# Performance work log

Hardware: AMD Instinct MI355X
Metric: run time of the kernel (lower is better)

Reference implementation:

```python
import jax, jax.numpy as jnp
import numpy as np

D_MODEL = 1024
D_STATE = 16
D_CONV = 4
EXPAND = 2
D_INNER = EXPAND * D_MODEL
DT_RANK = -(-D_MODEL // 16)  # ceil(d_model/16) = 64
LN_EPS = 1e-5


def setup_inputs() -> dict:
    key = jax.random.key(0)
    ks = jax.random.split(key, 10)
    b, l = 1, 2048
    s = 0.02
    x = jax.random.normal(ks[0], (b, l, D_MODEL), dtype=jnp.float32)
    gamma = jnp.ones((D_MODEL,), jnp.float32)
    beta = jnp.zeros((D_MODEL,), jnp.float32)
    w_in = jax.random.normal(ks[1], (2 * D_INNER, D_MODEL), jnp.float32) * s
    conv_w = jax.random.normal(ks[2], (D_INNER, D_CONV), jnp.float32) * s
    conv_b = jnp.zeros((D_INNER,), jnp.float32)
    w_x = jax.random.normal(ks[3], (DT_RANK + 2 * D_STATE, D_INNER), jnp.float32) * s
    w_dt = jax.random.normal(ks[4], (D_INNER, DT_RANK), jnp.float32) * s
    b_dt = jax.random.normal(ks[5], (D_INNER,), jnp.float32) * s
    A_log = jnp.log(jnp.broadcast_to(jnp.arange(1, D_STATE + 1, dtype=jnp.float32)[None, :], (D_INNER, D_STATE)))
    Dp = jnp.ones((D_INNER,), jnp.float32)
    w_out = jax.random.normal(ks[6], (D_MODEL, D_INNER), jnp.float32) * s
    return {"x": x, "gamma": gamma, "beta": beta, "w_in": w_in, "conv_w": conv_w,
            "conv_b": conv_b, "w_x": w_x, "w_dt": w_dt, "b_dt": b_dt,
            "A_log": A_log, "Dp": Dp, "w_out": w_out}


def _combine(e1, e2):
    # (a2, b2) o (a1, b1) = (a2*a1, a2*b1 + b2); e2 is the later element
    a1, b1 = e1
    a2, b2 = e2
    return (a2 * a1, a2 * b1 + b2)


def _forward(x, gamma, beta, w_in, conv_w, conv_b, w_x, w_dt, b_dt, A_log, Dp, w_out):
    residual = x
    # LayerNorm
    mu = jnp.mean(x, axis=-1, keepdims=True)
    var = jnp.var(x, axis=-1, keepdims=True)
    xn = (x - mu) * jax.lax.rsqrt(var + LN_EPS) * gamma + beta
    # in_proj and split
    xz = jnp.einsum('bld,ed->ble', xn, w_in)
    x_part, z = xz[..., :D_INNER], xz[..., D_INNER:]
    # causal depthwise conv1d (torch pads k-1 both sides then trims to l == left pad)
    lhs = jnp.transpose(x_part, (0, 2, 1))  # (b, d_inner, l)
    rhs = conv_w[:, None, :]                # (d_inner, 1, k)
    conv = jax.lax.conv_general_dilated(
        lhs, rhs, window_strides=(1,), padding=[(D_CONV - 1, 0)],
        dimension_numbers=('NCH', 'OIH', 'NCH'), feature_group_count=D_INNER)
    x_part = jnp.transpose(conv, (0, 2, 1)) + conv_b  # (b, l, d_inner)
    x_part = jax.nn.silu(x_part)  # dropout is identity in eval mode
    # SSM
    A = -jnp.exp(A_log)  # (d_inner, n)
    x_dbl = jnp.einsum('bld,ed->ble', x_part, w_x)
    dt = x_dbl[..., :DT_RANK]
    B = x_dbl[..., DT_RANK:DT_RANK + D_STATE]
    C = x_dbl[..., DT_RANK + D_STATE:]
    delta = jax.nn.softplus(jnp.einsum('blr,dr->bld', dt, w_dt) + b_dt)  # (b,l,d_inner)
    deltaA = jnp.exp(delta[..., None] * A[None, None])                    # (b,l,d_inner,n)
    dBu = delta[..., None] * B[:, :, None, :] * x_part[..., None]         # (b,l,d_inner,n)
    _, h = jax.lax.associative_scan(_combine, (deltaA, dBu), axis=1)
    y = jnp.sum(h * C[:, :, None, :], axis=-1) + x_part * Dp             # (b,l,d_inner)
    y = y * jax.nn.silu(z)
    out = jnp.einsum('ble,de->bld', y, w_out) + residual
    return out


def reference(x, gamma, beta, w_in, conv_w, conv_b, w_x, w_dt, b_dt, A_log, Dp, w_out):
    return _forward(x, gamma, beta, w_in, conv_w, conv_b, w_x, w_dt, b_dt, A_log, Dp, w_out)
```

## Files before the change

### kernel.cpp

```cpp
#include <hip/hip_runtime.h>
#include <math.h>

#define L_SEQ 2048
#define DM 1024
#define DI 2048
#define DS 16
#define DR 64
#define XDN 96
#define NCHUNK 64
#define TCH 32
#define KSLICES 8
#define KSL (DI / KSLICES)

typedef __attribute__((ext_vector_type(8))) short bf16x8;
typedef __attribute__((ext_vector_type(4))) float f32x4;
typedef unsigned short ushort_t;
typedef __attribute__((address_space(1))) const unsigned int GU32;
typedef __attribute__((address_space(3))) unsigned int LU32;

__device__ inline unsigned short f2bf(float f) {
  unsigned int u = __builtin_bit_cast(unsigned int, f);
  u += 0x7fffu + ((u >> 16) & 1u);
  return (unsigned short)(u >> 16);
}
__device__ inline float bf2f(unsigned short u) {
  return __builtin_bit_cast(float, (unsigned int)u << 16);
}

__device__ inline void cvt4(const float* src, ushort_t* dst, int j) {
  float4 v = ((const float4*)src)[j];
  ushort4 o;
  o.x = f2bf(v.x); o.y = f2bf(v.y); o.z = f2bf(v.z); o.w = f2bf(v.w);
  ((ushort4*)dst)[j] = o;
}

__global__ void cvt_all_kernel(const float* __restrict__ w_in,
                               const float* __restrict__ w_out,
                               const float* __restrict__ w_x,
                               const float* __restrict__ w_dt,
                               ushort_t* __restrict__ w_inb,
                               ushort_t* __restrict__ w_outb,
                               ushort_t* __restrict__ w_xb,
                               ushort_t* __restrict__ w_dtb) {
  int i = blockIdx.x * 256 + threadIdx.x;
  const int N0 = 2 * DI * DM / 4;
  const int N1 = N0 + DM * DI / 4;
  const int N2 = N1 + 128 * DI / 4;
  const int N3 = N2 + DI * DR / 4;
  if (i < N0) {
    cvt4(w_in, w_inb, i);
  } else if (i < N1) {
    cvt4(w_out, w_outb, i - N0);
  } else if (i < N2) {
    int j = i - N1;
    int e0 = j << 2;
    int row = e0 >> 11;
    int col = e0 & (DI - 1);
    ushort4 o = {0, 0, 0, 0};
    if (row < XDN) {
      float4 v = *(const float4*)(w_x + (size_t)row * DI + col);
      o.x = f2bf(v.x); o.y = f2bf(v.y); o.z = f2bf(v.z); o.w = f2bf(v.w);
    }
    ((ushort4*)w_xb)[j] = o;
  } else if (i < N3) {
    cvt4(w_dt, w_dtb, i - N2);
  }
}

__global__ void ln_kernel(const float* __restrict__ x,
                          const float* __restrict__ gamma,
                          const float* __restrict__ beta,
                          ushort_t* __restrict__ xnb) {
  int row = blockIdx.x;
  int t = threadIdx.x;
  const float4* xr = (const float4*)(x + (size_t)row * DM);
  float4 v = xr[t];
  float s = v.x + v.y + v.z + v.w;
  float s2 = v.x * v.x + v.y * v.y + v.z * v.z + v.w * v.w;
#pragma unroll
  for (int off = 32; off > 0; off >>= 1) {
    s += __shfl_down(s, off);
    s2 += __shfl_down(s2, off);
  }
  __shared__ float ls[4], ls2[4];
  if ((t & 63) == 0) { ls[t >> 6] = s; ls2[t >> 6] = s2; }
  __syncthreads();
  float tot = ls[0] + ls[1] + ls[2] + ls[3];
  float tot2 = ls2[0] + ls2[1] + ls2[2] + ls2[3];
  float mu = tot * (1.0f / DM);
  float var = tot2 * (1.0f / DM) - mu * mu;
  float r = rsqrtf(var + 1e-5f);
  float4 g = ((const float4*)gamma)[t];
  float4 b = ((const float4*)beta)[t];
  ushort4 o;
  o.x = f2bf((v.x - mu) * r * g.x + b.x);
  o.y = f2bf((v.y - mu) * r * g.y + b.y);
  o.z = f2bf((v.z - mu) * r * g.z + b.z);
  o.w = f2bf((v.w - mu) * r * g.w + b.w);
  ((ushort4*)(xnb + (size_t)row * DM))[t] = o;
}

template <int EPI>
__global__ __launch_bounds__(256) void mgemm(
    const ushort_t* __restrict__ A, int lda,
    const ushort_t* __restrict__ B, int ldb,
    void* __restrict__ Cp, int ldc, int ksl,
    const float* __restrict__ extra) {
  __shared__ ushort_t As[2][128 * 64];
  __shared__ ushort_t Bs[2][128 * 64];
  const int tid = threadIdx.x;
  const int lane = tid & 63;
  const int wave = tid >> 6;
  const int m0 = blockIdx.y * 128;
  const int n0 = blockIdx.x * 128;
  const int kbase = blockIdx.z * ksl;
  const int wr = (wave >> 1) * 64;
  const int wc = (wave & 1) * 64;
  const int kq = lane >> 4;
  const int rr = lane & 15;
  f32x4 acc[4][4];
#pragma unroll
  for (int i = 0; i < 4; ++i)
#pragma unroll
    for (int j = 0; j < 4; ++j) acc[i][j] = (f32x4){0.f, 0.f, 0.f, 0.f};

  int ur[4], uc[4];
#pragma unroll
  for (int q = 0; q < 4; ++q) {
    int u = tid + 256 * q;
    ur[q] = u >> 3;
    uc[q] = (((u & 7) ^ (ur[q] & 7)) << 3);
  }

#define STAGE(K0, S)                                                          \
  do {                                                                        \
    _Pragma("unroll") for (int q = 0; q < 4; ++q)                             \
        __builtin_amdgcn_global_load_lds(                                     \
            (GU32*)(A + (size_t)(m0 + ur[q]) * lda + (K0) + uc[q]),           \
            (LU32*)(&As[S][0] + (tid + 256 * q) * 8), 16, 0, 0);              \
    _Pragma("unroll") for (int q = 0; q < 4; ++q)                             \
        __builtin_amdgcn_global_load_lds(                                     \
            (GU32*)(B + (size_t)(n0 + ur[q]) * ldb + (K0) + uc[q]),           \
            (LU32*)(&Bs[S][0] + (tid + 256 * q) * 8), 16, 0, 0);              \
  } while (0)

  const int nk = ksl >> 6;
  STAGE(kbase, 0);
  for (int t = 0; t < nk; ++t) {
    const int cur = t & 1;
    if (t + 1 < nk) {
      STAGE(kbase + (t + 1) * 64, cur ^ 1);
      asm volatile("s_waitcnt vmcnt(8)" ::: "memory");
    } else {
      asm volatile("s_waitcnt vmcnt(0)" ::: "memory");
    }
    __builtin_amdgcn_s_barrier();
#pragma unroll
    for (int kk = 0; kk < 2; ++kk) {
      const int sw = ((rr & 7) << 4);
      bf16x8 a[4], b[4];
#pragma unroll
      for (int i = 0; i < 4; ++i) {
        int row = wr + i * 16 + rr;
        int off = ((kk * 64 + kq * 16) ^ sw);
        a[i] = *(const bf16x8*)((const char*)&As[cur][0] + row * 128 + off);
      }
#pragma unroll
      for (int j = 0; j < 4; ++j) {
        int row = wc + j * 16 + rr;
        int off = ((kk * 64 + kq * 16) ^ sw);
        b[j] = *(const bf16x8*)((const char*)&Bs[cur][0] + row * 128 + off);
      }
#pragma unroll
      for (int i = 0; i < 4; ++i)
#pragma unroll
        for (int j = 0; j < 4; ++j)
          acc[i][j] = __builtin_amdgcn_mfma_f32_16x16x32_bf16(a[i], b[j], acc[i][j], 0, 0, 0);
    }
    __builtin_amdgcn_s_barrier();
  }
#undef STAGE

#pragma unroll
  for (int i = 0; i < 4; ++i) {
#pragma unroll
    for (int j = 0; j < 4; ++j) {
#pragma unroll
      for (int r = 0; r < 4; ++r) {
        int row = m0 + wr + i * 16 + kq * 4 + r;
        int col = n0 + wc + j * 16 + rr;
        float v = acc[i][j][r];
        if (EPI == 4) {
          ((ushort_t*)Cp)[(size_t)row * ldc + col] = f2bf(v);
        } else if (EPI == 5) {
          v += extra[col];
          v = (v > 20.f) ? v : __logf(1.f + __expf(v));
          ((ushort_t*)Cp)[(size_t)row * ldc + col] = f2bf(v);
        } else if (EPI == 6) {
          ((float*)Cp)[((size_t)blockIdx.z * L_SEQ + row) * ldc + col] = v;
        }
      }
    }
  }
}

__global__ void reduce_xdbl_kernel(const float* __restrict__ part,
                                   float* __restrict__ xdbl,
                                   ushort_t* __restrict__ dtb) {
  int i = blockIdx.x * 256 + threadIdx.x;
  int col = i & 127;
  int row = i >> 7;
  float s = 0.f;
#pragma unroll
  for (int k = 0; k < KSLICES; ++k) s += part[(size_t)k * (L_SEQ * 128) + i];
  if (col < DR) dtb[(size_t)row * DR + col] = f2bf(s);
  if (col < XDN) xdbl[(size_t)row * XDN + col] = s;
}

__global__ void reduce_out_kernel(const float* __restrict__ part,
                                  const float* __restrict__ x,
                                  float* __restrict__ out) {
  int i = blockIdx.x * 256 + threadIdx.x;
  float4 p0 = ((const float4*)part)[i];
  float4 p1 = ((const float4*)(part + (size_t)L_SEQ * DM))[i];
  float4 xr = ((const float4*)x)[i];
  float4 o;
  o.x = p0.x + p1.x + xr.x;
  o.y = p0.y + p1.y + xr.y;
  o.z = p0.z + p1.z + xr.z;
  o.w = p0.w + p1.w + xr.w;
  ((float4*)out)[i] = o;
}

__global__ void conv_silu_kernel(const ushort_t* __restrict__ xzb,
                                 const float* __restrict__ conv_w,
                                 const float* __restrict__ conv_b,
                                 ushort_t* __restrict__ xconvb) {
  int i = blockIdx.x * blockDim.x + threadIdx.x;
  int d0 = (i & (DI / 4 - 1)) << 2;
  int t = i >> 9;
  float4 bia = *(const float4*)(conv_b + d0);
  float acc[4] = {bia.x, bia.y, bia.z, bia.w};
  float w[4][4];
#pragma unroll
  for (int c = 0; c < 4; ++c) {
    float4 wv = *(const float4*)(conv_w + (size_t)(d0 + c) * 4);
    w[c][0] = wv.x; w[c][1] = wv.y; w[c][2] = wv.z; w[c][3] = wv.w;
  }
#pragma unroll
  for (int j = 0; j < 4; ++j) {
    int tt = t - 3 + j;
    if (tt >= 0) {
      ushort4 xv = *(const ushort4*)(xzb + (size_t)tt * (2 * DI) + d0);
      acc[0] += bf2f(xv.x) * w[0][j];
      acc[1] += bf2f(xv.y) * w[1][j];
      acc[2] += bf2f(xv.z) * w[2][j];
      acc[3] += bf2f(xv.w) * w[3][j];
    }
  }
  ushort4 o;
  o.x = f2bf(acc[0] / (1.f + __expf(-acc[0])));
  o.y = f2bf(acc[1] / (1.f + __expf(-acc[1])));
  o.z = f2bf(acc[2] / (1.f + __expf(-acc[2])));
  o.w = f2bf(acc[3] / (1.f + __expf(-acc[3])));
  *(ushort4*)(xconvb + (size_t)t * DI + d0) = o;
}

__global__ void scan_chunk_kernel(const ushort_t* __restrict__ deltab,
                                  const ushort_t* __restrict__ ub,
                                  const float* __restrict__ xdbl,
                                  const float* __restrict__ A_log,
                                  float* __restrict__ P,
                                  float* __restrict__ HB) {
  int d = blockIdx.x * blockDim.x + threadIdx.x;
  int c = blockIdx.y;
  int t0 = c * TCH;
  float Aval[DS];
#pragma unroll
  for (int q = 0; q < 4; ++q) {
    float4 al = *(const float4*)(A_log + (size_t)d * DS + q * 4);
    Aval[q * 4 + 0] = -__expf(al.x);
    Aval[q * 4 + 1] = -__expf(al.y);
    Aval[q * 4 + 2] = -__expf(al.z);
    Aval[q * 4 + 3] = -__expf(al.w);
  }
  float h[DS], p[DS];
#pragma unroll
  for (int n = 0; n < DS; ++n) { h[n] = 0.f; p[n] = 1.f; }
  for (int t = t0; t < t0 + TCH; ++t) {
    float dlt = bf2f(deltab[(size_t)t * DI + d]);
    float uv = bf2f(ub[(size_t)t * DI + d]);
    float du = dlt * uv;
    float Bv[DS];
#pragma unroll
    for (int q = 0; q < 4; ++q) {
      float4 b4 = *(const float4*)(xdbl + (size_t)t * XDN + DR + q * 4);
      Bv[q * 4 + 0] = b4.x; Bv[q * 4 + 1] = b4.y;
      Bv[q * 4 + 2] = b4.z; Bv[q * 4 + 3] = b4.w;
    }
#pragma unroll
    for (int n = 0; n < DS; ++n) {
      float dA = __expf(dlt * Aval[n]);
      p[n] *= dA;
      h[n] = dA * h[n] + du * Bv[n];
    }
  }
#pragma unroll
  for (int n = 0; n < DS; ++n) {
    size_t idx = ((size_t)c * DS + n) * DI + d;
    P[idx] = p[n];
    HB[idx] = h[n];
  }
}

__global__ void scan_prop_kernel(const float* __restrict__ P,
                                 const float* __restrict__ HB,
                                 float* __restrict__ HIN) {
  int dn = blockIdx.x * blockDim.x + threadIdx.x;
  float h = 0.f;
#pragma unroll 4
  for (int c = 0; c < NCHUNK; ++c) {
    size_t idx = (size_t)c * (DI * DS) + dn;
    HIN[idx] = h;
    h = P[idx] * h + HB[idx];
  }
}

__global__ void scan_final_kernel(const ushort_t* __restrict__ deltab,
                                  const ushort_t* __restrict__ ub,
                                  const float* __restrict__ xdbl,
                                  const ushort_t* __restrict__ xzb,
                                  const float* __restrict__ A_log,
                                  const float* __restrict__ Dp,
                                  const float* __restrict__ HIN,
                                  ushort_t* __restrict__ ygb) {
  int d = blockIdx.x * blockDim.x + threadIdx.x;
  int c = blockIdx.y;
  int t0 = c * TCH;
  float Aval[DS];
#pragma unroll
  for (int q = 0; q < 4; ++q) {
    float4 al = *(const float4*)(A_log + (size_t)d * DS + q * 4);
    Aval[q * 4 + 0] = -__expf(al.x);
    Aval[q * 4 + 1] = -__expf(al.y);
    Aval[q * 4 + 2] = -__expf(al.z);
    Aval[q * 4 + 3] = -__expf(al.w);
  }
  float Dval = Dp[d];
  float h[DS];
#pragma unroll
  for (int n = 0; n < DS; ++n) h[n] = HIN[((size_t)c * DS + n) * DI + d];
  for (int t = t0; t < t0 + TCH; ++t) {
    float dlt = bf2f(deltab[(size_t)t * DI + d]);
    float uv = bf2f(ub[(size_t)t * DI + d]);
    float du = dlt * uv;
    float Bv[DS], Cv[DS];
#pragma unroll
    for (int q = 0; q < 4; ++q) {
      float4 b4 = *(const float4*)(xdbl + (size_t)t * XDN + DR + q * 4);
      float4 c4 = *(const float4*)(xdbl + (size_t)t * XDN + DR + DS + q * 4);
      Bv[q * 4 + 0] = b4.x; Bv[q * 4 + 1] = b4.y;
      Bv[q * 4 + 2] = b4.z; Bv[q * 4 + 3] = b4.w;
      Cv[q * 4 + 0] = c4.x; Cv[q * 4 + 1] = c4.y;
      Cv[q * 4 + 2] = c4.z; Cv[q * 4 + 3] = c4.w;
    }
    float acc = uv * Dval;
#pragma unroll
    for (int n = 0; n < DS; ++n) {
      float dA = __expf(dlt * Aval[n]);
      h[n] = dA * h[n] + du * Bv[n];
      acc += h[n] * Cv[n];
    }
    float z = bf2f(xzb[(size_t)t * (2 * DI) + DI + d]);
    float sz = z / (1.f + __expf(-z));
    ygb[(size_t)t * DI + d] = f2bf(acc * sz);
  }
}

extern "C" void kernel_launch(void* const* d_in, const int* in_sizes, int n_in,
                              void* d_out, int out_size, void* d_ws, size_t ws_size,
                              hipStream_t stream) {
  const float* x = (const float*)d_in[0];
  const float* gamma = (const float*)d_in[1];
  const float* beta = (const float*)d_in[2];
  const float* w_in = (const float*)d_in[3];
  const float* conv_w = (const float*)d_in[4];
  const float* conv_b = (const float*)d_in[5];
  const float* w_x = (const float*)d_in[6];
  const float* w_dt = (const float*)d_in[7];
  const float* b_dt = (const float*)d_in[8];
  const float* A_log = (const float*)d_in[9];
  const float* Dp = (const float*)d_in[10];
  const float* w_out = (const float*)d_in[11];
  float* out = (float*)d_out;

  float* ws = (float*)d_ws;
  float* xdbl = ws;
  float* P = xdbl + (size_t)L_SEQ * XDN;
  float* HB = P + (size_t)NCHUNK * DI * DS;
  float* HIN = HB + (size_t)NCHUNK * DI * DS;
  float* part = HIN + (size_t)NCHUNK * DI * DS;
  ushort_t* xzb = (ushort_t*)(part + (size_t)KSLICES * L_SEQ * 128);
  ushort_t* xconvb = xzb + (size_t)L_SEQ * 2 * DI;
  ushort_t* deltab = xconvb + (size_t)L_SEQ * DI;
  ushort_t* ygb = deltab + (size_t)L_SEQ * DI;
  ushort_t* xnb = ygb + (size_t)L_SEQ * DI;
  ushort_t* w_inb = xnb + (size_t)L_SEQ * DM;
  ushort_t* w_outb = w_inb + (size_t)(2 * DI) * DM;
  ushort_t* w_xb = w_outb + (size_t)DM * DI;
  ushort_t* w_dtb = w_xb + (size_t)128 * DI;
  ushort_t* dtb = w_dtb + (size_t)DI * DR;
  float* part_out = (float*)xzb;

  {
    int units = (2 * DI * DM + DM * DI + 128 * DI + DI * DR) / 4;
    cvt_all_kernel<<<(units + 255) / 256, 256, 0, stream>>>(
        w_in, w_out, w_x, w_dt, w_inb, w_outb, w_xb, w_dtb);
  }
  ln_kernel<<<L_SEQ, 256, 0, stream>>>(x, gamma, beta, xnb);
  mgemm<4><<<dim3((2 * DI) / 128, L_SEQ / 128, 1), 256, 0, stream>>>(
      xnb, DM, w_inb, DM, xzb, 2 * DI, DM, nullptr);
  conv_silu_kernel<<<(L_SEQ * DI / 4) / 256, 256, 0, stream>>>(
      xzb, conv_w, conv_b, xconvb);
  mgemm<6><<<dim3(1, L_SEQ / 128, KSLICES), 256, 0, stream>>>(
      xconvb, DI, w_xb, DI, part, 128, KSL, nullptr);
  reduce_xdbl_kernel<<<(L_SEQ * 128) / 256, 256, 0, stream>>>(part, xdbl, dtb);
  mgemm<5><<<dim3(DI / 128, L_SEQ / 128, 1), 256, 0, stream>>>(
      dtb, DR, w_dtb, DR, deltab, DI, DR, b_dt);
  scan_chunk_kernel<<<dim3(DI / 256, NCHUNK), 256, 0, stream>>>(
      deltab, xconvb, xdbl, A_log, P, HB);
  scan_prop_kernel<<<(DI * DS) / 256, 256, 0, stream>>>(P, HB, HIN);
  scan_final_kernel<<<dim3(DI / 256, NCHUNK), 256, 0, stream>>>(
      deltab, xconvb, xdbl, xzb, A_log, Dp, HIN, ygb);
  mgemm<6><<<dim3(DM / 128, L_SEQ / 128, 2), 256, 0, stream>>>(
      ygb, DI, w_outb, DI, part_out, DM, DI / 2, nullptr);
  reduce_out_kernel<<<(L_SEQ * DM / 4) / 256, 256, 0, stream>>>(part_out, x, out);
}
```

Baseline: 154.9 us.

## Use 8-wave GEMM blocks, fuse LayerNorm with weight conversion, retune chunking and split-K

The GEMM kernel now runs 512 threads (8 waves), each computing a 64x32 sub-tile instead of 64x64. This lowers accumulator register pressure and adds more waves to hide latency. The LayerNorm and weight-conversion kernels are merged into one launch. The scan chunk count is halved (longer chunks), and the out-projection split-K goes from 2 to 4 slices, which needs a separate partial buffer and a 4-way reduce. This adds more partial-sum traffic and longer serial chunk scans in exchange for more parallel GEMM blocks and fewer launches.

```diff
diff --git a/kernel.cpp b/kernel.cpp
--- a/kernel.cpp
+++ b/kernel.cpp
@@ -7,10 +7,11 @@
 #define DS 16
 #define DR 64
 #define XDN 96
-#define NCHUNK 64
-#define TCH 32
+#define NCHUNK 32
+#define TCH 64
 #define KSLICES 8
 #define KSL (DI / KSLICES)
+#define OSPLIT 4
 
 typedef __attribute__((ext_vector_type(8))) short bf16x8;
 typedef __attribute__((ext_vector_type(4))) float f32x4;
@@ -34,15 +35,49 @@
   ((ushort4*)dst)[j] = o;
 }
 
-__global__ void cvt_all_kernel(const float* __restrict__ w_in,
-                               const float* __restrict__ w_out,
-                               const float* __restrict__ w_x,
-                               const float* __restrict__ w_dt,
-                               ushort_t* __restrict__ w_inb,
-                               ushort_t* __restrict__ w_outb,
-                               ushort_t* __restrict__ w_xb,
-                               ushort_t* __restrict__ w_dtb) {
-  int i = blockIdx.x * 256 + threadIdx.x;
+__global__ void init_kernel(const float* __restrict__ x,
+                            const float* __restrict__ gamma,
+                            const float* __restrict__ beta,
+                            const float* __restrict__ w_in,
+                            const float* __restrict__ w_out,
+                            const float* __restrict__ w_x,
+                            const float* __restrict__ w_dt,
+                            ushort_t* __restrict__ xnb,
+                            ushort_t* __restrict__ w_inb,
+                            ushort_t* __restrict__ w_outb,
+                            ushort_t* __restrict__ w_xb,
+                            ushort_t* __restrict__ w_dtb) {
+  if (blockIdx.x < L_SEQ) {
+    int row = blockIdx.x;
+    int t = threadIdx.x;
+    const float4* xr = (const float4*)(x + (size_t)row * DM);
+    float4 v = xr[t];
+    float s = v.x + v.y + v.z + v.w;
+    float s2 = v.x * v.x + v.y * v.y + v.z * v.z + v.w * v.w;
+#pragma unroll
+    for (int off = 32; off > 0; off >>= 1) {
+      s += __shfl_down(s, off);
+      s2 += __shfl_down(s2, off);
+    }
+    __shared__ float ls[4], ls2[4];
+    if ((t & 63) == 0) { ls[t >> 6] = s; ls2[t >> 6] = s2; }
+    __syncthreads();
+    float tot = ls[0] + ls[1] + ls[2] + ls[3];
+    float tot2 = ls2[0] + ls2[1] + ls2[2] + ls2[3];
+    float mu = tot * (1.0f / DM);
+    float var = tot2 * (1.0f / DM) - mu * mu;
+    float r = rsqrtf(var + 1e-5f);
+    float4 g = ((const float4*)gamma)[t];
+    float4 b = ((const float4*)beta)[t];
+    ushort4 o;
+    o.x = f2bf((v.x - mu) * r * g.x + b.x);
+    o.y = f2bf((v.y - mu) * r * g.y + b.y);
+    o.z = f2bf((v.z - mu) * r * g.z + b.z);
+    o.w = f2bf((v.w - mu) * r * g.w + b.w);
+    ((ushort4*)(xnb + (size_t)row * DM))[t] = o;
+    return;
+  }
+  int i = (blockIdx.x - L_SEQ) * 256 + threadIdx.x;
   const int N0 = 2 * DI * DM / 4;
   const int N1 = N0 + DM * DI / 4;
   const int N2 = N1 + 128 * DI / 4;
@@ -67,41 +102,8 @@
   }
 }
 
-__global__ void ln_kernel(const float* __restrict__ x,
-                          const float* __restrict__ gamma,
-                          const float* __restrict__ beta,
-                          ushort_t* __restrict__ xnb) {
-  int row = blockIdx.x;
-  int t = threadIdx.x;
-  const float4* xr = (const float4*)(x + (size_t)row * DM);
-  float4 v = xr[t];
-  float s = v.x + v.y + v.z + v.w;
-  float s2 = v.x * v.x + v.y * v.y + v.z * v.z + v.w * v.w;
-#pragma unroll
-  for (int off = 32; off > 0; off >>= 1) {
-    s += __shfl_down(s, off);
-    s2 += __shfl_down(s2, off);
-  }
-  __shared__ float ls[4], ls2[4];
-  if ((t & 63) == 0) { ls[t >> 6] = s; ls2[t >> 6] = s2; }
-  __syncthreads();
-  float tot = ls[0] + ls[1] + ls[2] + ls[3];
-  float tot2 = ls2[0] + ls2[1] + ls2[2] + ls2[3];
-  float mu = tot * (1.0f / DM);
-  float var = tot2 * (1.0f / DM) - mu * mu;
-  float r = rsqrtf(var + 1e-5f);
-  float4 g = ((const float4*)gamma)[t];
-  float4 b = ((const float4*)beta)[t];
-  ushort4 o;
-  o.x = f2bf((v.x - mu) * r * g.x + b.x);
-  o.y = f2bf((v.y - mu) * r * g.y + b.y);
-  o.z = f2bf((v.z - mu) * r * g.z + b.z);
-  o.w = f2bf((v.w - mu) * r * g.w + b.w);
-  ((ushort4*)(xnb + (size_t)row * DM))[t] = o;
-}
-
 template <int EPI>
-__global__ __launch_bounds__(256) void mgemm(
+__global__ __launch_bounds__(512) void mgemm(
     const ushort_t* __restrict__ A, int lda,
     const ushort_t* __restrict__ B, int ldb,
     void* __restrict__ Cp, int ldc, int ksl,
@@ -114,34 +116,34 @@
   const int m0 = blockIdx.y * 128;
   const int n0 = blockIdx.x * 128;
   const int kbase = blockIdx.z * ksl;
-  const int wr = (wave >> 1) * 64;
-  const int wc = (wave & 1) * 64;
+  const int wr = (wave >> 2) * 64;
+  const int wc = (wave & 3) * 32;
   const int kq = lane >> 4;
   const int rr = lane & 15;
-  f32x4 acc[4][4];
+  f32x4 acc[4][2];
 #pragma unroll
   for (int i = 0; i < 4; ++i)
 #pragma unroll
-    for (int j = 0; j < 4; ++j) acc[i][j] = (f32x4){0.f, 0.f, 0.f, 0.f};
-
-  int ur[4], uc[4];
-#pragma unroll
-  for (int q = 0; q < 4; ++q) {
-    int u = tid + 256 * q;
+    for (int j = 0; j < 2; ++j) acc[i][j] = (f32x4){0.f, 0.f, 0.f, 0.f};
+
+  int ur[2], uc[2];
+#pragma unroll
+  for (int q = 0; q < 2; ++q) {
+    int u = tid + 512 * q;
     ur[q] = u >> 3;
     uc[q] = (((u & 7) ^ (ur[q] & 7)) << 3);
   }
 
 #define STAGE(K0, S)                                                          \
   do {                                                                        \
-    _Pragma("unroll") for (int q = 0; q < 4; ++q)                             \
+    _Pragma("unroll") for (int q = 0; q < 2; ++q)                             \
         __builtin_amdgcn_global_load_lds(                                     \
             (GU32*)(A + (size_t)(m0 + ur[q]) * lda + (K0) + uc[q]),           \
-            (LU32*)(&As[S][0] + (tid + 256 * q) * 8), 16, 0, 0);              \
-    _Pragma("unroll") for (int q = 0; q < 4; ++q)                             \
+            (LU32*)(&As[S][0] + (tid + 512 * q) * 8), 16, 0, 0);              \
+    _Pragma("unroll") for (int q = 0; q < 2; ++q)                             \
         __builtin_amdgcn_global_load_lds(                                     \
             (GU32*)(B + (size_t)(n0 + ur[q]) * ldb + (K0) + uc[q]),           \
-            (LU32*)(&Bs[S][0] + (tid + 256 * q) * 8), 16, 0, 0);              \
+            (LU32*)(&Bs[S][0] + (tid + 512 * q) * 8), 16, 0, 0);              \
   } while (0)
 
   const int nk = ksl >> 6;
@@ -150,7 +152,7 @@
     const int cur = t & 1;
     if (t + 1 < nk) {
       STAGE(kbase + (t + 1) * 64, cur ^ 1);
-      asm volatile("s_waitcnt vmcnt(8)" ::: "memory");
+      asm volatile("s_waitcnt vmcnt(4)" ::: "memory");
     } else {
       asm volatile("s_waitcnt vmcnt(0)" ::: "memory");
     }
@@ -158,7 +160,7 @@
 #pragma unroll
     for (int kk = 0; kk < 2; ++kk) {
       const int sw = ((rr & 7) << 4);
-      bf16x8 a[4], b[4];
+      bf16x8 a[4], b[2];
 #pragma unroll
       for (int i = 0; i < 4; ++i) {
         int row = wr + i * 16 + rr;
@@ -166,7 +168,7 @@
         a[i] = *(const bf16x8*)((const char*)&As[cur][0] + row * 128 + off);
       }
 #pragma unroll
-      for (int j = 0; j < 4; ++j) {
+      for (int j = 0; j < 2; ++j) {
         int row = wc + j * 16 + rr;
         int off = ((kk * 64 + kq * 16) ^ sw);
         b[j] = *(const bf16x8*)((const char*)&Bs[cur][0] + row * 128 + off);
@@ -174,7 +176,7 @@
 #pragma unroll
       for (int i = 0; i < 4; ++i)
 #pragma unroll
-        for (int j = 0; j < 4; ++j)
+        for (int j = 0; j < 2; ++j)
           acc[i][j] = __builtin_amdgcn_mfma_f32_16x16x32_bf16(a[i], b[j], acc[i][j], 0, 0, 0);
     }
     __builtin_amdgcn_s_barrier();
@@ -184,7 +186,7 @@
 #pragma unroll
   for (int i = 0; i < 4; ++i) {
 #pragma unroll
-    for (int j = 0; j < 4; ++j) {
+    for (int j = 0; j < 2; ++j) {
 #pragma unroll
       for (int r = 0; r < 4; ++r) {
         int row = m0 + wr + i * 16 + kq * 4 + r;
@@ -221,14 +223,13 @@
                                   const float* __restrict__ x,
                                   float* __restrict__ out) {
   int i = blockIdx.x * 256 + threadIdx.x;
-  float4 p0 = ((const float4*)part)[i];
-  float4 p1 = ((const float4*)(part + (size_t)L_SEQ * DM))[i];
   float4 xr = ((const float4*)x)[i];
-  float4 o;
-  o.x = p0.x + p1.x + xr.x;
-  o.y = p0.y + p1.y + xr.y;
-  o.z = p0.z + p1.z + xr.z;
-  o.w = p0.w + p1.w + xr.w;
+  float4 o = xr;
+#pragma unroll
+  for (int s = 0; s < OSPLIT; ++s) {
+    float4 p = ((const float4*)(part + (size_t)s * L_SEQ * DM))[i];
+    o.x += p.x; o.y += p.y; o.z += p.z; o.w += p.w;
+  }
   ((float4*)out)[i] = o;
 }
 
@@ -400,7 +401,8 @@
   float* HB = P + (size_t)NCHUNK * DI * DS;
   float* HIN = HB + (size_t)NCHUNK * DI * DS;
   float* part = HIN + (size_t)NCHUNK * DI * DS;
-  ushort_t* xzb = (ushort_t*)(part + (size_t)KSLICES * L_SEQ * 128);
+  float* part_out = part + (size_t)KSLICES * L_SEQ * 128;
+  ushort_t* xzb = (ushort_t*)(part_out + (size_t)OSPLIT * L_SEQ * DM);
   ushort_t* xconvb = xzb + (size_t)L_SEQ * 2 * DI;
   ushort_t* deltab = xconvb + (size_t)L_SEQ * DI;
   ushort_t* ygb = deltab + (size_t)L_SEQ * DI;
@@ -410,29 +412,28 @@
   ushort_t* w_xb = w_outb + (size_t)DM * DI;
   ushort_t* w_dtb = w_xb + (size_t)128 * DI;
   ushort_t* dtb = w_dtb + (size_t)DI * DR;
-  float* part_out = (float*)xzb;
 
   {
     int units = (2 * DI * DM + DM * DI + 128 * DI + DI * DR) / 4;
-    cvt_all_kernel<<<(units + 255) / 256, 256, 0, stream>>>(
-        w_in, w_out, w_x, w_dt, w_inb, w_outb, w_xb, w_dtb);
-  }
-  ln_kernel<<<L_SEQ, 256, 0, stream>>>(x, gamma, beta, xnb);
-  mgemm<4><<<dim3((2 * DI) / 128, L_SEQ / 128, 1), 256, 0, stream>>>(
+    int nblk = L_SEQ + (units + 255) / 256;
+    init_kernel<<<nblk, 256, 0, stream>>>(
+        x, gamma, beta, w_in, w_out, w_x, w_dt, xnb, w_inb, w_outb, w_xb, w_dtb);
+  }
+  mgemm<4><<<dim3((2 * DI) / 128, L_SEQ / 128, 1), 512, 0, stream>>>(
       xnb, DM, w_inb, DM, xzb, 2 * DI, DM, nullptr);
   conv_silu_kernel<<<(L_SEQ * DI / 4) / 256, 256, 0, stream>>>(
       xzb, conv_w, conv_b, xconvb);
-  mgemm<6><<<dim3(1, L_SEQ / 128, KSLICES), 256, 0, stream>>>(
+  mgemm<6><<<dim3(1, L_SEQ / 128, KSLICES), 512, 0, stream>>>(
       xconvb, DI, w_xb, DI, part, 128, KSL, nullptr);
   reduce_xdbl_kernel<<<(L_SEQ * 128) / 256, 256, 0, stream>>>(part, xdbl, dtb);
-  mgemm<5><<<dim3(DI / 128, L_SEQ / 128, 1), 256, 0, stream>>>(
+  mgemm<5><<<dim3(DI / 128, L_SEQ / 128, 1), 512, 0, stream>>>(
       dtb, DR, w_dtb, DR, deltab, DI, DR, b_dt);
   scan_chunk_kernel<<<dim3(DI / 256, NCHUNK), 256, 0, stream>>>(
       deltab, xconvb, xdbl, A_log, P, HB);
   scan_prop_kernel<<<(DI * DS) / 256, 256, 0, stream>>>(P, HB, HIN);
   scan_final_kernel<<<dim3(DI / 256, NCHUNK), 256, 0, stream>>>(
       deltab, xconvb, xdbl, xzb, A_log, Dp, HIN, ygb);
-  mgemm<6><<<dim3(DM / 128, L_SEQ / 128, 2), 256, 0, stream>>>(
-      ygb, DI, w_outb, DI, part_out, DM, DI / 2, nullptr);
+  mgemm<6><<<dim3(DM / 128, L_SEQ / 128, OSPLIT), 512, 0, stream>>>(
+      ygb, DI, w_outb, DI, part_out, DM, DI / OSPLIT, nullptr);
   reduce_out_kernel<<<(L_SEQ * DM / 4) / 256, 256, 0, stream>>>(part_out, x, out);
 }
```

Result: slower. 163.3 us (+5.4%).
